# Kernel tuning notes

Hardware: AMD Instinct MI355X
Metric: run time of the kernel (lower is better)

Reference implementation:

```python
import jax, jax.numpy as jnp
import numpy as np

DIM = 192
NUM_HEADS = 6
WS = 7            # window_size
SS = 3            # shift_size
MLP_HIDDEN = int(DIM * 4.0)
HEAD_DIM = DIM // NUM_HEADS
SCALE = HEAD_DIM ** -0.5
N = WS * WS


def _relative_position_index(ws):
    coords = np.stack(np.meshgrid(np.arange(ws), np.arange(ws), indexing='ij'))  # [2,ws,ws]
    cf = coords.reshape(2, -1)
    rel = cf[:, :, None] - cf[:, None, :]          # [2,N,N]
    rel = rel.transpose(1, 2, 0).copy()
    rel[:, :, 0] += ws - 1
    rel[:, :, 1] += ws - 1
    rel[:, :, 0] *= 2 * ws - 1
    return rel.sum(-1)                              # [N,N]

RPI = jnp.asarray(_relative_position_index(WS))


def _attn_mask(Hp, Wp, ws, ss):
    img = np.zeros((Hp, Wp))
    cnt = 0
    slices = (slice(0, -ws), slice(-ws, -ss), slice(-ss, None))
    for h in slices:
        for w in slices:
            img[h, w] = cnt
            cnt += 1
    mw = img.reshape(Hp // ws, ws, Wp // ws, ws).transpose(0, 2, 1, 3).reshape(-1, ws * ws)
    am = mw[:, None, :] - mw[:, :, None]            # [nWins,N,N]
    am = np.where(am != 0, -100.0, 0.0).astype(np.float32)
    return jnp.asarray(am)


def _layernorm(x, g, b, eps=1e-5):
    mu = jnp.mean(x, axis=-1, keepdims=True)
    var = jnp.mean(jnp.square(x - mu), axis=-1, keepdims=True)
    return (x - mu) * jax.lax.rsqrt(var + eps) * g + b


def setup_inputs() -> dict:
    key = jax.random.key(0)
    ks = jax.random.split(key, 16)
    s = lambda k, shp, sc=0.02: jax.random.normal(k, shp, jnp.float32) * sc
    return {
        'x': jax.random.normal(ks[0], (32, 3136, DIM), jnp.float32),
        'qkv_w': s(ks[1], (DIM, 3 * DIM)),
        'qkv_b': jnp.zeros((3 * DIM,), jnp.float32),
        'proj_w': s(ks[2], (DIM, DIM)),
        'proj_b': jnp.zeros((DIM,), jnp.float32),
        'rpb_table': s(ks[3], ((2 * WS - 1) * (2 * WS - 1), NUM_HEADS)),
        'ln1_g': jnp.ones((DIM,), jnp.float32),
        'ln1_b': jnp.zeros((DIM,), jnp.float32),
        'ln2_g': jnp.ones((DIM,), jnp.float32),
        'ln2_b': jnp.zeros((DIM,), jnp.float32),
        'w1': s(ks[4], (DIM, MLP_HIDDEN)),
        'b1': jnp.zeros((MLP_HIDDEN,), jnp.float32),
        'w2': s(ks[5], (MLP_HIDDEN, DIM)),
        'b2': jnp.zeros((DIM,), jnp.float32),
        'H': 56,
        'W': 56,
    }


def reference(x, qkv_w, qkv_b, proj_w, proj_b, rpb_table, ln1_g, ln1_b,
              ln2_g, ln2_b, w1, b1, w2, b2, H, W):
    B, L, C = x.shape
    shortcut = x
    h = _layernorm(x, ln1_g, ln1_b).reshape(B, H, W, C)

    pad_r = (WS - W % WS) % WS
    pad_b = (WS - H % WS) % WS
    h = jnp.pad(h, ((0, 0), (0, pad_b), (0, pad_r), (0, 0)))
    Hp, Wp = H + pad_b, W + pad_r
    nH, nW = Hp // WS, Wp // WS
    nWins = nH * nW

    if SS > 0:
        h = jnp.roll(h, shift=(-SS, -SS), axis=(1, 2))
        attn_mask = _attn_mask(Hp, Wp, WS, SS)       # [nWins,N,N]
    else:
        attn_mask = None

    # window partition -> [B*nWins, N, C]
    win = h.reshape(B, nH, WS, nW, WS, C).transpose(0, 1, 3, 2, 4, 5)
    win = win.reshape(B * nWins, N, C)

    # attention
    qkv = win @ qkv_w + qkv_b                        # [B_,N,3C]
    qkv = qkv.reshape(-1, N, 3, NUM_HEADS, HEAD_DIM).transpose(2, 0, 3, 1, 4)
    q, k, v = qkv[0] * SCALE, qkv[1], qkv[2]         # [B_,h,N,d]
    attn = jnp.einsum('bhnd,bhmd->bhnm', q, k)

    rpb = rpb_table[RPI.reshape(-1)].reshape(N, N, NUM_HEADS).transpose(2, 0, 1)
    attn = attn + rpb[None]
    if attn_mask is not None:
        attn = attn.reshape(B, nWins, NUM_HEADS, N, N) + attn_mask[None, :, None]
        attn = attn.reshape(-1, NUM_HEADS, N, N)
    attn = jax.nn.softmax(attn, axis=-1)
    out = jnp.einsum('bhnm,bhmd->bhnd', attn, v).transpose(0, 2, 1, 3).reshape(-1, N, C)
    out = out @ proj_w + proj_b

    # window reverse
    out = out.reshape(B, nH, nW, WS, WS, C).transpose(0, 1, 3, 2, 4, 5).reshape(B, Hp, Wp, C)
    if SS > 0:
        out = jnp.roll(out, shift=(SS, SS), axis=(1, 2))
    if pad_r > 0 or pad_b > 0:
        out = out[:, :H, :W, :]
    out = out.reshape(B, H * W, C)

    h = shortcut + out
    ff = _layernorm(h, ln2_g, ln2_b)
    ff = jax.nn.gelu(ff @ w1 + b1, approximate=False) @ w2 + b2
    return h + ff
```

## Files before the change

### kernel.cpp

```cpp
#include <hip/hip_runtime.h>
#include <hip/hip_bf16.h>
#include <cstdint>

typedef __hip_bfloat16 bf16;
typedef __attribute__((ext_vector_type(4))) float f32x4;
typedef __attribute__((ext_vector_type(8))) __bf16 bf16x8;

#define SCALE 0.17677669529663687f

#define OFF_WTQ   0
#define OFF_WTP   221184
#define OFF_WT1   294912
#define OFF_WT2   589824
#define OFF_RMAP  884736
#define OFF_A     1286144
#define OFF_B     39821312
#define OFF_C     193961984

__global__ __launch_bounds__(256) void prep_k(
    const float* __restrict__ qkv_w, const float* __restrict__ proj_w,
    const float* __restrict__ w1, const float* __restrict__ w2,
    bf16* __restrict__ wtq, bf16* __restrict__ wtp,
    bf16* __restrict__ wt1, bf16* __restrict__ wt2, int* __restrict__ rmap)
{
  int i = blockIdx.x * 256 + threadIdx.x;
  if (i < 110592) {
    int n = i / 192, k = i - n * 192;
    wtq[i] = __float2bfloat16(qkv_w[k * 576 + n]);
  } else if (i < 147456) {
    int j = i - 110592; int n = j / 192, k = j - n * 192;
    wtp[j] = __float2bfloat16(proj_w[k * 192 + n]);
  } else if (i < 294912) {
    int j = i - 147456; int n = j / 192, k = j - n * 192;
    wt1[j] = __float2bfloat16(w1[k * 768 + n]);
  } else if (i < 442368) {
    int j = i - 294912; int n = j / 768, k = j - n * 768;
    wt2[j] = __float2bfloat16(w2[k * 192 + n]);
  } else if (i < 542720) {
    int m = i - 442368;
    int win = m / 49, nn = m - win * 49;
    int b = win >> 6, iw = win & 63;
    int wh = iw >> 3, ww = iw & 7;
    int ty = nn / 7, tx = nn - ty * 7;
    int rr = wh * 7 + ty + 3; if (rr >= 56) rr -= 56;
    int cc = ww * 7 + tx + 3; if (cc >= 56) cc -= 56;
    rmap[m] = b * 3136 + rr * 56 + cc;
  }
}

template<bool MAP>
__global__ __launch_bounds__(256) void ln_k(
    const float* __restrict__ x, const float* __restrict__ g,
    const float* __restrict__ b, const int* __restrict__ rmap,
    bf16* __restrict__ out)
{
  int wv = threadIdx.x >> 6, lane = threadIdx.x & 63;
  long m = (long)blockIdx.x * 4 + wv;
  long src = MAP ? (long)rmap[m] : m;
  const float* row = x + src * 192;
  float v0 = row[lane], v1 = row[lane + 64], v2 = row[lane + 128];
  float s = v0 + v1 + v2;
  #pragma unroll
  for (int d = 1; d < 64; d <<= 1) s += __shfl_xor(s, d, 64);
  float mu = s * (1.0f / 192.0f);
  float d0 = v0 - mu, d1 = v1 - mu, d2 = v2 - mu;
  float q = d0 * d0 + d1 * d1 + d2 * d2;
  #pragma unroll
  for (int d = 1; d < 64; d <<= 1) q += __shfl_xor(q, d, 64);
  float inv = 1.0f / sqrtf(q * (1.0f / 192.0f) + 1e-5f);
  bf16* o = out + m * 192;
  o[lane]       = __float2bfloat16(d0 * inv * g[lane]       + b[lane]);
  o[lane + 64]  = __float2bfloat16(d1 * inv * g[lane + 64]  + b[lane + 64]);
  o[lane + 128] = __float2bfloat16(d2 * inv * g[lane + 128] + b[lane + 128]);
}

template<int MODE, int KD>
__global__ __launch_bounds__(256) void gemm_k(
    const bf16* __restrict__ A, const bf16* __restrict__ Bt,
    const float* __restrict__ bias, const float* __restrict__ extra,
    const int* __restrict__ rmap, void* __restrict__ outp)
{
  __shared__ bf16 As[128 * 64];
  const int tid = threadIdx.x;
  const int lane = tid & 63;
  const int w = tid >> 6;
  const int wm = w >> 1, wn = w & 1;
  const long m0 = (long)blockIdx.y * 128;
  const int n0 = blockIdx.x * 64;
  const int r = lane & 15, kb = lane >> 4;

  f32x4 acc[4][2];
  #pragma unroll
  for (int a = 0; a < 4; ++a)
    #pragma unroll
    for (int bb = 0; bb < 2; ++bb) acc[a][bb] = (f32x4){0.f, 0.f, 0.f, 0.f};

  for (int k0 = 0; k0 < KD; k0 += 64) {
    #pragma unroll
    for (int it = 0; it < 4; ++it) {
      int li = tid + it * 256;
      int m = li >> 3;
      int sl = (li & 7) ^ (m & 7);
      const bf16* src = A + (m0 + m) * KD + k0 + sl * 8;
      bf16* dst = As + (size_t)(w * 64 + it * 256) * 8;
      __builtin_amdgcn_global_load_lds(
          (const __attribute__((address_space(1))) unsigned int*)src,
          (__attribute__((address_space(3))) unsigned int*)dst, 16, 0, 0);
    }
    __syncthreads();

    bf16x8 af[2][4], bfr[2][2];
    #pragma unroll
    for (int h2 = 0; h2 < 2; ++h2) {
      #pragma unroll
      for (int mi = 0; mi < 4; ++mi) {
        int m = wm * 64 + mi * 16 + r;
        int slot = (h2 * 4 + kb) ^ (r & 7);
        af[h2][mi] = *(const bf16x8*)(As + m * 64 + slot * 8);
      }
      #pragma unroll
      for (int ni = 0; ni < 2; ++ni) {
        int n = n0 + wn * 32 + ni * 16 + r;
        bfr[h2][ni] = *(const bf16x8*)(Bt + (long)n * KD + k0 + h2 * 32 + kb * 8);
      }
    }
    #pragma unroll
    for (int h2 = 0; h2 < 2; ++h2)
      #pragma unroll
      for (int mi = 0; mi < 4; ++mi)
        #pragma unroll
        for (int ni = 0; ni < 2; ++ni)
          acc[mi][ni] = __builtin_amdgcn_mfma_f32_16x16x32_bf16(
              af[h2][mi], bfr[h2][ni], acc[mi][ni], 0, 0, 0);
    __syncthreads();
  }

  #pragma unroll
  for (int mi = 0; mi < 4; ++mi) {
    #pragma unroll
    for (int ni = 0; ni < 2; ++ni) {
      int col = n0 + wn * 32 + ni * 16 + r;
      float bb = bias[col];
      #pragma unroll
      for (int rr = 0; rr < 4; ++rr) {
        long row = m0 + wm * 64 + mi * 16 + kb * 4 + rr;
        float c = acc[mi][ni][rr] + bb;
        if constexpr (MODE == 0) {
          ((bf16*)outp)[row * 576 + col] = __float2bfloat16(c);
        } else if constexpr (MODE == 1) {
          long gr = rmap[row];
          ((float*)outp)[gr * 192 + col] = extra[gr * 192 + col] + c;
        } else if constexpr (MODE == 2) {
          float ge = 0.5f * c * (1.0f + erff(c * 0.70710678118654752f));
          ((bf16*)outp)[row * 768 + col] = __float2bfloat16(ge);
        } else {
          ((float*)outp)[row * 192 + col] = extra[row * 192 + col] + c;
        }
      }
    }
  }
}

__global__ __launch_bounds__(64) void attn_k(
    const bf16* __restrict__ qkv, const float* __restrict__ rpb,
    bf16* __restrict__ aout)
{
  __shared__ bf16 P[64 * 72];
  __shared__ bf16 Vt[32 * 72];
  int lane = threadIdx.x;
  int r = lane & 15, kb = lane >> 4;
  int head = blockIdx.x % 6;
  int win = blockIdx.x / 6;
  int iw = win & 63;
  int wh = iw >> 3, ww = iw & 7;
  const bf16* base = qkv + (long)win * (49 * 576);

  bf16x8 qf[4], kf[4];
  #pragma unroll
  for (int t = 0; t < 4; ++t) {
    int row = t * 16 + r;
    if (row < 49) {
      qf[t] = *(const bf16x8*)(base + row * 576 + head * 32 + kb * 8);
      kf[t] = *(const bf16x8*)(base + row * 576 + 192 + head * 32 + kb * 8);
    } else {
      qf[t] = (bf16x8){0, 0, 0, 0, 0, 0, 0, 0};
      kf[t] = (bf16x8){0, 0, 0, 0, 0, 0, 0, 0};
    }
  }
  f32x4 zero = {0.f, 0.f, 0.f, 0.f};
  f32x4 s[4][4];
  #pragma unroll
  for (int ti = 0; ti < 4; ++ti)
    #pragma unroll
    for (int tj = 0; tj < 4; ++tj)
      s[ti][tj] = __builtin_amdgcn_mfma_f32_16x16x32_bf16(qf[ti], kf[tj], zero, 0, 0, 0);

  {
    int j = lane;
    if (j < 49) {
      #pragma unroll
      for (int d0 = 0; d0 < 32; d0 += 8) {
        bf16x8 v8 = *(const bf16x8*)(base + j * 576 + 384 + head * 32 + d0);
        #pragma unroll
        for (int u = 0; u < 8; ++u) Vt[(d0 + u) * 72 + j] = *((const bf16*)&v8 + u);
      }
    } else {
      for (int d = 0; d < 32; ++d) Vt[d * 72 + j] = __float2bfloat16(0.0f);
    }
  }

  #pragma unroll
  for (int ti = 0; ti < 4; ++ti) {
    #pragma unroll
    for (int rr = 0; rr < 4; ++rr) {
      int i = ti * 16 + kb * 4 + rr;
      int ii = i < 49 ? i : 48;
      int yi = ii / 7, xi = ii - yi * 7;
      int ari = wh * 7 + yi, aci = ww * 7 + xi;
      int gi = (ari < 49 ? 0 : (ari < 53 ? 1 : 2)) * 3 + (aci < 49 ? 0 : (aci < 53 ? 1 : 2));
      float vals[4];
      #pragma unroll
      for (int tj = 0; tj < 4; ++tj) {
        int j = tj * 16 + r;
        int jj = j < 49 ? j : 48;
        int yj = jj / 7, xj = jj - yj * 7;
        float pb = rpb[((yi - yj + 6) * 13 + (xi - xj + 6)) * 6 + head];
        int arj = wh * 7 + yj, acj = ww * 7 + xj;
        int gj = (arj < 49 ? 0 : (arj < 53 ? 1 : 2)) * 3 + (acj < 49 ? 0 : (acj < 53 ? 1 : 2));
        float v = s[ti][tj][rr] * SCALE + pb;
        if (gi != gj) v -= 100.0f;
        if (i >= 49 || j >= 49) v = -1e30f;
        vals[tj] = v;
      }
      float mx = fmaxf(fmaxf(vals[0], vals[1]), fmaxf(vals[2], vals[3]));
      #pragma unroll
      for (int d = 1; d < 16; d <<= 1) mx = fmaxf(mx, __shfl_xor(mx, d, 64));
      float e0 = __expf(vals[0] - mx), e1 = __expf(vals[1] - mx);
      float e2 = __expf(vals[2] - mx), e3 = __expf(vals[3] - mx);
      float sum = e0 + e1 + e2 + e3;
      #pragma unroll
      for (int d = 1; d < 16; d <<= 1) sum += __shfl_xor(sum, d, 64);
      float inv = 1.0f / sum;
      P[i * 72 + 0  + r] = __float2bfloat16(e0 * inv);
      P[i * 72 + 16 + r] = __float2bfloat16(e1 * inv);
      P[i * 72 + 32 + r] = __float2bfloat16(e2 * inv);
      P[i * 72 + 48 + r] = __float2bfloat16(e3 * inv);
    }
  }
  __syncthreads();

  f32x4 o[4][2];
  #pragma unroll
  for (int ti = 0; ti < 4; ++ti)
    #pragma unroll
    for (int dt = 0; dt < 2; ++dt) o[ti][dt] = zero;
  #pragma unroll
  for (int kt = 0; kt < 2; ++kt) {
    bf16x8 pf[4], vf[2];
    #pragma unroll
    for (int ti = 0; ti < 4; ++ti)
      pf[ti] = *(const bf16x8*)(P + (ti * 16 + r) * 72 + kt * 32 + kb * 8);
    #pragma unroll
    for (int dt = 0; dt < 2; ++dt)
      vf[dt] = *(const bf16x8*)(Vt + (dt * 16 + r) * 72 + kt * 32 + kb * 8);
    #pragma unroll
    for (int ti = 0; ti < 4; ++ti)
      #pragma unroll
      for (int dt = 0; dt < 2; ++dt)
        o[ti][dt] = __builtin_amdgcn_mfma_f32_16x16x32_bf16(pf[ti], vf[dt], o[ti][dt], 0, 0, 0);
  }
  #pragma unroll
  for (int ti = 0; ti < 4; ++ti)
    #pragma unroll
    for (int dt = 0; dt < 2; ++dt)
      #pragma unroll
      for (int rr = 0; rr < 4; ++rr) {
        int i = ti * 16 + kb * 4 + rr;
        if (i < 49)
          aout[((long)win * 49 + i) * 192 + head * 32 + dt * 16 + r] =
              __float2bfloat16(o[ti][dt][rr]);
      }
}

extern "C" void kernel_launch(void* const* d_in, const int* in_sizes, int n_in,
                              void* d_out, int out_size, void* d_ws, size_t ws_size,
                              hipStream_t stream)
{
  const float* x      = (const float*)d_in[0];
  const float* qkv_w  = (const float*)d_in[1];
  const float* qkv_b  = (const float*)d_in[2];
  const float* proj_w = (const float*)d_in[3];
  const float* proj_b = (const float*)d_in[4];
  const float* rpb    = (const float*)d_in[5];
  const float* ln1_g  = (const float*)d_in[6];
  const float* ln1_b  = (const float*)d_in[7];
  const float* ln2_g  = (const float*)d_in[8];
  const float* ln2_b  = (const float*)d_in[9];
  const float* w1     = (const float*)d_in[10];
  const float* b1     = (const float*)d_in[11];
  const float* w2     = (const float*)d_in[12];
  const float* b2     = (const float*)d_in[13];

  char* ws = (char*)d_ws;
  bf16* wtq = (bf16*)(ws + OFF_WTQ);
  bf16* wtp = (bf16*)(ws + OFF_WTP);
  bf16* wt1 = (bf16*)(ws + OFF_WT1);
  bf16* wt2 = (bf16*)(ws + OFF_WT2);
  int*  rmap = (int*)(ws + OFF_RMAP);
  bf16* Abuf = (bf16*)(ws + OFF_A);
  bf16* Bbuf = (bf16*)(ws + OFF_B);
  float* hbuf = (float*)(ws + OFF_C);

  prep_k<<<2120, 256, 0, stream>>>(qkv_w, proj_w, w1, w2, wtq, wtp, wt1, wt2, rmap);
  ln_k<true><<<25088, 256, 0, stream>>>(x, ln1_g, ln1_b, rmap, Abuf);
  gemm_k<0, 192><<<dim3(9, 784), 256, 0, stream>>>(Abuf, wtq, qkv_b, nullptr, nullptr, Bbuf);
  attn_k<<<12288, 64, 0, stream>>>(Bbuf, rpb, Abuf);
  gemm_k<1, 192><<<dim3(3, 784), 256, 0, stream>>>(Abuf, wtp, proj_b, x, rmap, hbuf);
  ln_k<false><<<25088, 256, 0, stream>>>(hbuf, ln2_g, ln2_b, nullptr, Abuf);
  gemm_k<2, 192><<<dim3(12, 784), 256, 0, stream>>>(Abuf, wt1, b1, nullptr, nullptr, Bbuf);
  gemm_k<3, 768><<<dim3(3, 784), 256, 0, stream>>>(Bbuf, wt2, b2, hbuf, nullptr, (float*)d_out);
}
```

Before: 581.3 us.

## Fuse LayerNorm2, fc1, GELU and fc2 into one MLP kernel

Replaces the separate LN2 kernel and the two MLP GEMM launches with a single kernel. Each 64-row block normalizes its rows into LDS, then works through the 768-wide hidden layer in four 192-column chunks, staging each GELU chunk in LDS and accumulating fc2 into registers. This removes the global write and re-read of the normalized activations and the large bf16 hidden tensor, plus two launches. In exchange, B-operand fragments of both weight matrices are read from global/L2 by every block with no LDS staging, the two 64x196 LDS buffers may limit occupancy, and exact erf GELU is replaced by a tanh-style exp approximation.

After: 633.8 us. 1.09x slower.

```diff
diff --git a/kernel.cpp b/kernel.cpp
--- a/kernel.cpp
+++ b/kernel.cpp
@@ -147,15 +147,133 @@
         float c = acc[mi][ni][rr] + bb;
         if constexpr (MODE == 0) {
           ((bf16*)outp)[row * 576 + col] = __float2bfloat16(c);
-        } else if constexpr (MODE == 1) {
+        } else {
           long gr = rmap[row];
           ((float*)outp)[gr * 192 + col] = extra[gr * 192 + col] + c;
-        } else if constexpr (MODE == 2) {
-          float ge = 0.5f * c * (1.0f + erff(c * 0.70710678118654752f));
-          ((bf16*)outp)[row * 768 + col] = __float2bfloat16(ge);
-        } else {
-          ((float*)outp)[row * 192 + col] = extra[row * 192 + col] + c;
         }
+      }
+    }
+  }
+}
+
+#define LPAD 196
+__global__ __launch_bounds__(256) void mlp_k(
+    const float* __restrict__ h, const float* __restrict__ g2,
+    const float* __restrict__ bg2, const bf16* __restrict__ w1t,
+    const float* __restrict__ b1, const bf16* __restrict__ w2t,
+    const float* __restrict__ b2, float* __restrict__ outp)
+{
+  __shared__ bf16 Al[64 * LPAD];
+  __shared__ bf16 Hl[64 * LPAD];
+  const int tid = threadIdx.x;
+  const int lane = tid & 63, w = tid >> 6;
+  const int wm = w >> 1, wn = w & 1;
+  const int r = lane & 15, kb = lane >> 4;
+  const long m0 = (long)blockIdx.x * 64;
+
+  {
+    float gv0 = g2[lane], gv1 = g2[lane + 64], gv2 = g2[lane + 128];
+    float bv0 = bg2[lane], bv1 = bg2[lane + 64], bv2 = bg2[lane + 128];
+    #pragma unroll
+    for (int half = 0; half < 2; ++half) {
+      float va[8][3];
+      #pragma unroll
+      for (int i = 0; i < 8; ++i) {
+        const float* row = h + (m0 + w * 16 + half * 8 + i) * 192;
+        va[i][0] = row[lane]; va[i][1] = row[lane + 64]; va[i][2] = row[lane + 128];
+      }
+      #pragma unroll
+      for (int i = 0; i < 8; ++i) {
+        float s = va[i][0] + va[i][1] + va[i][2];
+        #pragma unroll
+        for (int d = 1; d < 64; d <<= 1) s += __shfl_xor(s, d, 64);
+        float mu = s * (1.0f / 192.0f);
+        float d0 = va[i][0] - mu, d1 = va[i][1] - mu, d2 = va[i][2] - mu;
+        float q = d0 * d0 + d1 * d1 + d2 * d2;
+        #pragma unroll
+        for (int d = 1; d < 64; d <<= 1) q += __shfl_xor(q, d, 64);
+        float inv = 1.0f / sqrtf(q * (1.0f / 192.0f) + 1e-5f);
+        bf16* o = Al + (w * 16 + half * 8 + i) * LPAD;
+        o[lane]       = __float2bfloat16(d0 * inv * gv0 + bv0);
+        o[lane + 64]  = __float2bfloat16(d1 * inv * gv1 + bv1);
+        o[lane + 128] = __float2bfloat16(d2 * inv * gv2 + bv2);
+      }
+    }
+  }
+  __syncthreads();
+
+  f32x4 oacc[2][6];
+  #pragma unroll
+  for (int mi = 0; mi < 2; ++mi)
+    #pragma unroll
+    for (int nj = 0; nj < 6; ++nj) oacc[mi][nj] = (f32x4){0.f, 0.f, 0.f, 0.f};
+
+  for (int c = 0; c < 4; ++c) {
+    f32x4 hacc[2][6];
+    #pragma unroll
+    for (int mi = 0; mi < 2; ++mi)
+      #pragma unroll
+      for (int nj = 0; nj < 6; ++nj) hacc[mi][nj] = (f32x4){0.f, 0.f, 0.f, 0.f};
+
+    #pragma unroll
+    for (int ks = 0; ks < 6; ++ks) {
+      bf16x8 af[2], bfr[6];
+      #pragma unroll
+      for (int mi = 0; mi < 2; ++mi)
+        af[mi] = *(const bf16x8*)(Al + (wm * 32 + mi * 16 + r) * LPAD + ks * 32 + kb * 8);
+      #pragma unroll
+      for (int nj = 0; nj < 6; ++nj)
+        bfr[nj] = *(const bf16x8*)(w1t + (c * 192 + wn * 96 + nj * 16 + r) * 192 + ks * 32 + kb * 8);
+      #pragma unroll
+      for (int mi = 0; mi < 2; ++mi)
+        #pragma unroll
+        for (int nj = 0; nj < 6; ++nj)
+          hacc[mi][nj] = __builtin_amdgcn_mfma_f32_16x16x32_bf16(af[mi], bfr[nj], hacc[mi][nj], 0, 0, 0);
+    }
+    #pragma unroll
+    for (int nj = 0; nj < 6; ++nj) {
+      float b1v = b1[c * 192 + wn * 96 + nj * 16 + r];
+      #pragma unroll
+      for (int mi = 0; mi < 2; ++mi) {
+        #pragma unroll
+        for (int rr = 0; rr < 4; ++rr) {
+          float xv = hacc[mi][nj][rr] + b1v;
+          float t = __expf(fmaf(0.0713548162f * xv, xv * xv, 1.5957692f * xv));
+          float ge = xv * t / (t + 1.0f);
+          Hl[(wm * 32 + mi * 16 + kb * 4 + rr) * LPAD + wn * 96 + nj * 16 + r] = __float2bfloat16(ge);
+        }
+      }
+    }
+    __syncthreads();
+
+    #pragma unroll
+    for (int ks = 0; ks < 6; ++ks) {
+      bf16x8 af2[2], bf2[6];
+      #pragma unroll
+      for (int mi = 0; mi < 2; ++mi)
+        af2[mi] = *(const bf16x8*)(Hl + (wm * 32 + mi * 16 + r) * LPAD + ks * 32 + kb * 8);
+      #pragma unroll
+      for (int nj = 0; nj < 6; ++nj)
+        bf2[nj] = *(const bf16x8*)(w2t + (wn * 96 + nj * 16 + r) * 768 + c * 192 + ks * 32 + kb * 8);
+      #pragma unroll
+      for (int mi = 0; mi < 2; ++mi)
+        #pragma unroll
+        for (int nj = 0; nj < 6; ++nj)
+          oacc[mi][nj] = __builtin_amdgcn_mfma_f32_16x16x32_bf16(af2[mi], bf2[nj], oacc[mi][nj], 0, 0, 0);
+    }
+    __syncthreads();
+  }
+
+  #pragma unroll
+  for (int mi = 0; mi < 2; ++mi) {
+    #pragma unroll
+    for (int nj = 0; nj < 6; ++nj) {
+      int col = wn * 96 + nj * 16 + r;
+      float b2v = b2[col];
+      #pragma unroll
+      for (int rr = 0; rr < 4; ++rr) {
+        long row = m0 + wm * 32 + mi * 16 + kb * 4 + rr;
+        outp[row * 192 + col] = h[row * 192 + col] + oacc[mi][nj][rr] + b2v;
       }
     }
   }
@@ -316,7 +434,5 @@
   gemm_k<0, 192><<<dim3(9, 784), 256, 0, stream>>>(Abuf, wtq, qkv_b, nullptr, nullptr, Bbuf);
   attn_k<<<12288, 64, 0, stream>>>(Bbuf, rpb, Abuf);
   gemm_k<1, 192><<<dim3(3, 784), 256, 0, stream>>>(Abuf, wtp, proj_b, x, rmap, hbuf);
-  ln_k<false><<<25088, 256, 0, stream>>>(hbuf, ln2_g, ln2_b, nullptr, Abuf);
-  gemm_k<2, 192><<<dim3(12, 784), 256, 0, stream>>>(Abuf, wt1, b1, nullptr, nullptr, Bbuf);
-  gemm_k<3, 768><<<dim3(3, 784), 256, 0, stream>>>(Bbuf, wt2, b2, hbuf, nullptr, (float*)d_out);
-}
+  mlp_k<<<1568, 256, 0, stream>>>(hbuf, ln2_g, ln2_b, wt1, b1, wt2, b2, (float*)d_out);
+}
```
